# Kernel tuning notes

Hardware: AMD Instinct MI355X
Metric: run time of the kernel (lower is better)

## Reference

```python
import jax, jax.numpy as jnp
import numpy as np
import math

B, T, C, H = 2, 2048, 1024, 16
D = C // H

def setup_inputs() -> dict:
    key = jax.random.key(0)
    ks = jax.random.split(key, 10)
    s = 1.0 / math.sqrt(C)
    return {
        "x": jax.random.normal(ks[0], (B, T, C), jnp.float32),
        "x_query": jax.random.normal(ks[1], (B, T, C), jnp.float32),
        "Wq": jax.random.normal(ks[2], (C, C), jnp.float32) * s,
        "bq": jax.random.normal(ks[3], (C,), jnp.float32) * 0.02,
        "Wk": jax.random.normal(ks[4], (C, C), jnp.float32) * s,
        "bk": jax.random.normal(ks[5], (C,), jnp.float32) * 0.02,
        "Wv": jax.random.normal(ks[6], (C, C), jnp.float32) * s,
        "bv": jax.random.normal(ks[7], (C,), jnp.float32) * 0.02,
        "Wp": jax.random.normal(ks[8], (C, C), jnp.float32) * s,
        "bp": jax.random.normal(ks[9], (C,), jnp.float32) * 0.02,
    }

def reference(x, x_query, Wq, bq, Wk, bk, Wv, bv, Wp, bp):
    # torch nn.Linear: y = x @ W^T + b
    Tq = x_query.shape[1]
    Tk = x.shape[1]
    q = (x_query @ Wq.T + bq).reshape(B, Tq, H, D).transpose(0, 2, 1, 3)  # [B,H,Tq,D]
    k = (x @ Wk.T + bk).reshape(B, Tk, H, D).transpose(0, 2, 1, 3)       # [B,H,Tk,D]
    v = (x @ Wv.T + bv).reshape(B, Tk, H, D).transpose(0, 2, 1, 3)       # [B,H,Tk,D]
    scale = 1.0 / math.sqrt(D)
    att = jnp.einsum('bhqd,bhkd->bhqk', q, k) * scale                    # [B,H,Tq,Tk]
    # use_mask=True, past_kv=None -> causal tril mask over (Tq, Tk)
    mask = jnp.tril(jnp.ones((Tq, Tk), dtype=bool))
    att = jnp.where(mask[None, None, :, :], att, -jnp.inf)
    att = jax.nn.softmax(att, axis=-1)
    y = jnp.einsum('bhqk,bhkd->bhqd', att, v)                            # [B,H,Tq,D]
    y = y.transpose(0, 2, 1, 3).reshape(B, Tq, C)
    y = y @ Wp.T + bp
    return y
```

## Files before the change

kernel.cpp:

```cpp
#include <hip/hip_runtime.h>

typedef __bf16 bf16;
typedef __attribute__((ext_vector_type(8))) __bf16 bf16x8;
typedef __attribute__((ext_vector_type(4))) float f32x4;
typedef __attribute__((ext_vector_type(16))) float f32x16;
typedef __attribute__((ext_vector_type(4))) unsigned u32x4;

#define MFMA16(a, b, c) __builtin_amdgcn_mfma_f32_16x16x32_bf16((a), (b), (c), 0, 0, 0)
#define MFMA32(a, b, c) __builtin_amdgcn_mfma_f32_32x32x16_bf16((a), (b), (c), 0, 0, 0)
#define NEG_BIG (-1e30f)
#define SCL_LOG2 0.18033688011112042f
#define THR_RAW 44.3614195558365f

__device__ __forceinline__ void gload_lds16(void* lds, const void* g) {
  __builtin_amdgcn_global_load_lds(
      (const __attribute__((address_space(1))) void*)g,
      (__attribute__((address_space(3))) void*)lds, 16, 0, 0);
}

__device__ __forceinline__ unsigned pk2(float x, float y) {
  const unsigned short a = __builtin_bit_cast(unsigned short, (bf16)x);
  const unsigned short b = __builtin_bit_cast(unsigned short, (bf16)y);
  return (unsigned)a | ((unsigned)b << 16);
}

static __device__ const signed char KQT[32] =
  {15,15,10,10, 15,14,14,14,13, 9, 9, 4, 13,13,12,12, 8, 8,
   12,11,11,11, 7, 7, 3,  6, 6,  5, 5, 2,  1,  0};
static __device__ const signed char KSEG[32] =
  { 0, 1, 0, 1,  2, 0, 1, 2, 0, 0, 1, 0,  1, 2, 0, 1, 0, 1,
    2, 0, 1, 2, 0, 1, 0,  0, 1,  0, 1, 0,  0,  0};

__global__ void cvt6(const float* __restrict__ s0, const float* __restrict__ s1,
                     const float* __restrict__ s2, const float* __restrict__ s3,
                     const float* __restrict__ s4, const float* __restrict__ s5,
                     bf16* __restrict__ d0, bf16* __restrict__ d1,
                     bf16* __restrict__ d2, bf16* __restrict__ d3,
                     bf16* __restrict__ d4, bf16* __restrict__ d5) {
  const int c = blockIdx.x * blockDim.x + threadIdx.x;
  if (c >= 1572864) return;
  const float* s; bf16* d; int off;
  if (c < 524288)        { s = s0; d = d0; off = c; }
  else if (c < 1048576)  { s = s1; d = d1; off = c - 524288; }
  else {
    const int c2 = c - 1048576, seg = c2 >> 17;
    off = c2 & 131071;
    s = seg == 0 ? s2 : seg == 1 ? s3 : seg == 2 ? s4 : s5;
    d = seg == 0 ? d2 : seg == 1 ? d3 : seg == 2 ? d4 : d5;
  }
  const float4 a = ((const float4*)s)[off * 2 + 0];
  const float4 b = ((const float4*)s)[off * 2 + 1];
  bf16x8 o;
  o[0] = (bf16)a.x; o[1] = (bf16)a.y; o[2] = (bf16)a.z; o[3] = (bf16)a.w;
  o[4] = (bf16)b.x; o[5] = (bf16)b.y; o[6] = (bf16)b.z; o[7] = (bf16)b.w;
  ((bf16x8*)d)[off] = o;
}

__global__ void gemm_qkv(const bf16* __restrict__ XQ, const bf16* __restrict__ X,
                         const bf16* __restrict__ Wq, const bf16* __restrict__ Wk,
                         const bf16* __restrict__ Wv,
                         const float* __restrict__ bq, const float* __restrict__ bk,
                         const float* __restrict__ bv,
                         bf16* __restrict__ Qo, bf16* __restrict__ Ko,
                         bf16* __restrict__ Vto) {
  __shared__ __align__(16) char As[128 * 128];
  __shared__ __align__(16) char Bs[128 * 128];
  const int tid = threadIdx.x;
  const int wv = tid >> 6, lane = tid & 63;
  const int wr = wv >> 1, wc = wv & 1;
  const int lr = lane & 15, lg = lane >> 4;
  const int seg = blockIdx.x >> 3;
  const int n0 = (blockIdx.x & 7) * 128;
  const int m0 = blockIdx.y * 128;
  const bf16* __restrict__ A = seg == 0 ? XQ : X;
  const bf16* __restrict__ W = seg == 0 ? Wq : seg == 1 ? Wk : Wv;
  const float* __restrict__ bias = seg == 0 ? bq : seg == 1 ? bk : bv;
  const int K = 1024;

  f32x4 acc[4][4] = {};

  for (int k0 = 0; k0 < K; k0 += 64) {
    __syncthreads();
#pragma unroll
    for (int j = 0; j < 4; ++j) {
      const int c = j * 256 + tid;
      const int row = c >> 3, cc = c & 7;
      const int gcol = (cc ^ (row & 7)) * 8;
      gload_lds16(As + (j * 256 + wv * 64) * 16,
                  A + (size_t)(m0 + row) * K + k0 + gcol);
      gload_lds16(Bs + (j * 256 + wv * 64) * 16,
                  W + (size_t)(n0 + row) * K + k0 + gcol);
    }
    __syncthreads();
#pragma unroll
    for (int half = 0; half < 2; ++half) {
      const int kb = half * 64 + lg * 16;
      bf16x8 af[4], bfr[4];
#pragma unroll
      for (int i = 0; i < 4; ++i) {
        const int row = wr * 64 + i * 16 + lr;
        af[i] = *(const bf16x8*)(As + row * 128 + (kb ^ ((row & 7) << 4)));
      }
#pragma unroll
      for (int j = 0; j < 4; ++j) {
        const int row = wc * 64 + j * 16 + lr;
        bfr[j] = *(const bf16x8*)(Bs + row * 128 + (kb ^ ((row & 7) << 4)));
      }
#pragma unroll
      for (int i = 0; i < 4; ++i)
#pragma unroll
        for (int j = 0; j < 4; ++j)
          acc[i][j] = MFMA16(af[i], bfr[j], acc[i][j]);
    }
  }

#pragma unroll
  for (int j = 0; j < 4; ++j) {
    const int n = n0 + wc * 64 + j * 16 + lr;
    const float bvv = bias[n];
    const int h = n >> 6, d = n & 63;
#pragma unroll
    for (int i = 0; i < 4; ++i) {
#pragma unroll
      for (int r = 0; r < 4; ++r) {
        const int m = m0 + wr * 64 + i * 16 + lg * 4 + r;
        const float v = acc[i][j][r] + bvv;
        const int b = m >> 11, t = m & 2047;
        if (seg == 0)      Qo[((size_t)(b * 16 + h) * 2048 + t) * 64 + d] = (bf16)v;
        else if (seg == 1) Ko[((size_t)(b * 16 + h) * 2048 + t) * 64 + d] = (bf16)v;
        else               Vto[((size_t)(b * 16 + h) * 64 + d) * 2048 + t] = (bf16)v;
      }
    }
  }
}

__global__ void gemm_out(const bf16* __restrict__ A, const bf16* __restrict__ W,
                         const float* __restrict__ bias, float* __restrict__ out,
                         int M, int N, int K) {
  __shared__ __align__(16) char As[128 * 128];
  __shared__ __align__(16) char Bs[64 * 128];
  const int tid = threadIdx.x;
  const int wv = tid >> 6, lane = tid & 63;
  const int wr = wv >> 1, wc = wv & 1;
  const int lr = lane & 15, lg = lane >> 4;
  const int m0 = blockIdx.y * 128, n0 = blockIdx.x * 64;

  f32x4 acc[4][2] = {};

  for (int k0 = 0; k0 < K; k0 += 64) {
    __syncthreads();
#pragma unroll
    for (int j = 0; j < 4; ++j) {
      const int c = j * 256 + tid;
      const int row = c >> 3, cc = c & 7;
      const int gcol = (cc ^ (row & 7)) * 8;
      gload_lds16(As + (j * 256 + wv * 64) * 16,
                  A + (size_t)(m0 + row) * K + k0 + gcol);
    }
#pragma unroll
    for (int j = 0; j < 2; ++j) {
      const int c = j * 256 + tid;
      const int row = c >> 3, cc = c & 7;
      const int gcol = (cc ^ (row & 7)) * 8;
      gload_lds16(Bs + (j * 256 + wv * 64) * 16,
                  W + (size_t)(n0 + row) * K + k0 + gcol);
    }
    __syncthreads();
#pragma unroll
    for (int half = 0; half < 2; ++half) {
      const int kb = half * 64 + lg * 16;
      bf16x8 af[4], bfr[2];
#pragma unroll
      for (int i = 0; i < 4; ++i) {
        const int row = wr * 64 + i * 16 + lr;
        af[i] = *(const bf16x8*)(As + row * 128 + (kb ^ ((row & 7) << 4)));
      }
#pragma unroll
      for (int j = 0; j < 2; ++j) {
        const int row = wc * 32 + j * 16 + lr;
        bfr[j] = *(const bf16x8*)(Bs + row * 128 + (kb ^ ((row & 7) << 4)));
      }
#pragma unroll
      for (int i = 0; i < 4; ++i)
#pragma unroll
        for (int j = 0; j < 2; ++j)
          acc[i][j] = MFMA16(af[i], bfr[j], acc[i][j]);
    }
  }

#pragma unroll
  for (int j = 0; j < 2; ++j) {
    const int n = n0 + wc * 32 + j * 16 + lr;
    const float bv = bias[n];
#pragma unroll
    for (int i = 0; i < 4; ++i) {
#pragma unroll
      for (int r = 0; r < 4; ++r) {
        const int m = m0 + wr * 64 + i * 16 + lg * 4 + r;
        out[(size_t)m * N + n] = acc[i][j][r] + bv;
      }
    }
  }
}

__global__ void attn_fwd(const bf16* __restrict__ Q, const bf16* __restrict__ Kk,
                         const bf16* __restrict__ Vt, bf16* __restrict__ attout,
                         bf16* __restrict__ Opart, float* __restrict__ Ml) {
  __shared__ __align__(16) char Ks[2][8192];
  __shared__ __align__(16) char Vs[2][8192];

  const int tid = threadIdx.x;
  const int wv = tid >> 6, lane = tid & 63;
  const int q31 = lane & 31, hi = lane >> 5, l7 = lane & 7;
  const int kind = blockIdx.x >> 5, bh = blockIdx.x & 31;
  const int qt = KQT[kind], seg = KSEG[kind];
  const int nt = 2 * qt + 2;
  const int ns = qt >= 11 ? 3 : (qt >= 5 ? 2 : 1);
  const int t0 = (nt * seg) / ns, t1 = (nt * (seg + 1)) / ns;
  const bool split = ns > 1;

  const int q0 = qt * 128;
  const int qs = q0 + wv * 32;
  const int qa = qs + q31;
  const size_t bhT = (size_t)bh * 2048;
  const bf16* Vh = Vt + (size_t)bh * 64 * 2048;

  bf16x8 qf[4];
#pragma unroll
  for (int kw = 0; kw < 4; ++kw)
    qf[kw] = *(const bf16x8*)(Q + (bhT + qa) * 64 + kw * 16 + hi * 8);

  u32x4 onesu; onesu[0] = onesu[1] = onesu[2] = onesu[3] = 0x3F803F80u;
  const bf16x8 ones8 = __builtin_bit_cast(bf16x8, onesu);

  f32x16 O0 = {}, O1 = {};
  f32x16 Ol = {};
  float m2 = NEG_BIG;

  auto STAGE = [&](int buf, int kv0) {
#pragma unroll
    for (int rr = 0; rr < 2; ++rr) {
      const int c = rr * 256 + tid;
      const int row = c >> 3, cc = c & 7;
      const int gcol = (cc ^ (row & 7)) * 8;
      gload_lds16(Ks[buf] + (rr * 256 + wv * 64) * 16,
                  Kk + (bhT + kv0 + row) * 64 + gcol);
      gload_lds16(Vs[buf] + (rr * 256 + wv * 64) * 16,
                  Vh + (size_t)row * 2048 + kv0 + gcol);
    }
  };

  STAGE(0, t0 * 64);
  __syncthreads();

  for (int it = t0; it < t1; ++it) {
    const int kv0 = it * 64;
    const int cur = (it - t0) & 1;
    if (it + 1 < t1) STAGE(cur ^ 1, (it + 1) * 64);

    if (kv0 <= qs + 31) {
      f32x16 S0 = {}, S1 = {};
      __builtin_amdgcn_s_setprio(1);
#pragma unroll
      for (int kw = 0; kw < 4; ++kw) {
        const int cb = (32 * kw + 16 * hi) ^ (l7 << 4);
        const bf16x8 k0 = *(const bf16x8*)(Ks[cur] + q31 * 128 + cb);
        const bf16x8 k1 = *(const bf16x8*)(Ks[cur] + (32 + q31) * 128 + cb);
        S0 = MFMA32(k0, qf[kw], S0);
        S1 = MFMA32(k1, qf[kw], S1);
      }
      __builtin_amdgcn_s_setprio(0);

      float p[32];
#pragma unroll
      for (int r = 0; r < 16; ++r) { p[r] = S0[r]; p[16 + r] = S1[r]; }
      if (kv0 + 63 > qs) {
#pragma unroll
        for (int a = 0; a < 2; ++a)
#pragma unroll
          for (int r = 0; r < 16; ++r) {
            const int kva = kv0 + a * 32 + (r & 3) + 8 * (r >> 2) + 4 * hi;
            if (kva > qa) p[a * 16 + r] = NEG_BIG;
          }
      }

      float w16[16];
#pragma unroll
      for (int i = 0; i < 16; ++i) w16[i] = fmaxf(p[i], p[i + 16]);
#pragma unroll
      for (int i = 0; i < 8; ++i) w16[i] = fmaxf(w16[i], w16[i + 8]);
#pragma unroll
      for (int i = 0; i < 4; ++i) w16[i] = fmaxf(w16[i], w16[i + 4]);
      float mx = fmaxf(fmaxf(w16[0], w16[1]), fmaxf(w16[2], w16[3]));
      mx = fmaxf(mx, __shfl_xor(mx, 32));
      if (!__all(mx - m2 <= THR_RAW)) {
        const float mnew = fmaxf(m2, mx);
        const float fac = exp2f((m2 - mnew) * SCL_LOG2);
#pragma unroll
        for (int r = 0; r < 16; ++r) { O0[r] *= fac; O1[r] *= fac; }
        Ol[0] *= fac;
        m2 = mnew;
      }
      const float nm2 = -m2 * SCL_LOG2;
#pragma unroll
      for (int i = 0; i < 32; ++i) p[i] = exp2f(__builtin_fmaf(p[i], SCL_LOG2, nm2));

      bf16x8 pf[4];
#pragma unroll
      for (int ks = 0; ks < 4; ++ks) {
        const int base = 16 * (ks >> 1) + 8 * (ks & 1);
        const unsigned g0 = pk2(p[base + 0], p[base + 1]);
        const unsigned g1 = pk2(p[base + 2], p[base + 3]);
        const unsigned g2 = pk2(p[base + 4], p[base + 5]);
        const unsigned g3 = pk2(p[base + 6], p[base + 7]);
        const unsigned e0 = __shfl_xor(hi ? g0 : g2, 32);
        const unsigned e1 = __shfl_xor(hi ? g1 : g3, 32);
        u32x4 w4;
        w4[0] = hi ? e0 : g0;
        w4[1] = hi ? e1 : g1;
        w4[2] = hi ? g2 : e0;
        w4[3] = hi ? g3 : e1;
        pf[ks] = __builtin_bit_cast(bf16x8, w4);
      }

      __builtin_amdgcn_s_setprio(1);
#pragma unroll
      for (int ks = 0; ks < 4; ++ks) {
        const int cb = (32 * ks + 16 * hi) ^ (l7 << 4);
        const bf16x8 v0 = *(const bf16x8*)(Vs[cur] + q31 * 128 + cb);
        const bf16x8 v1 = *(const bf16x8*)(Vs[cur] + (32 + q31) * 128 + cb);
        O0 = MFMA32(v0, pf[ks], O0);
        O1 = MFMA32(v1, pf[ks], O1);
        Ol = MFMA32(ones8, pf[ks], Ol);
      }
      __builtin_amdgcn_s_setprio(0);
    }
    __syncthreads();
  }

  const float l = Ol[0];
  if (!split) {
    const int b = bh >> 4, h = bh & 15;
    const float inv = 1.f / l;
    bf16* orow = attout + ((size_t)b * 2048 + qa) * 1024 + h * 64;
#pragma unroll
    for (int r = 0; r < 16; ++r) {
      const int dd = (r & 3) + 8 * (r >> 2) + 4 * hi;
      orow[dd]      = (bf16)(O0[r] * inv);
      orow[32 + dd] = (bf16)(O1[r] * inv);
    }
  } else {
    const int sbase = (qt < 11) ? (qt - 5) * 2 : 12 + (qt - 11) * 3;
    const int slot = bh * 27 + sbase + seg;
    bf16* Po = Opart + (size_t)slot * 8192;
    const int row = wv * 32 + q31;
#pragma unroll
    for (int r = 0; r < 16; ++r) {
      const int dd = (r & 3) + 8 * (r >> 2) + 4 * hi;
      Po[row * 64 + dd]      = (bf16)O0[r];
      Po[row * 64 + 32 + dd] = (bf16)O1[r];
    }
    Ml[slot * 256 + row]       = m2;
    Ml[slot * 256 + 128 + row] = l;
  }
}

__global__ void attn_combine(const bf16* __restrict__ Opart,
                             const float* __restrict__ Ml,
                             bf16* __restrict__ attout) {
  const int u = blockIdx.x;
  const int bh = u / 11, qti = u - bh * 11;
  const int qt = qti + 5;
  const int ns = qt >= 11 ? 3 : 2;
  const int sbase = (qt < 11) ? (qt - 5) * 2 : 12 + (qt - 11) * 3;
  const int s0 = bh * 27 + sbase;
  const int tid = threadIdx.x;
  const int row = tid >> 1, c0 = (tid & 1) * 32;

  float m[3], lv[3];
  float M = NEG_BIG;
#pragma unroll
  for (int s = 0; s < 3; ++s)
    if (s < ns) {
      m[s] = Ml[(s0 + s) * 256 + row];
      lv[s] = Ml[(s0 + s) * 256 + 128 + row];
      M = fmaxf(M, m[s]);
    }
  float w[3], L = 0.f;
#pragma unroll
  for (int s = 0; s < 3; ++s)
    if (s < ns) {
      w[s] = exp2f((m[s] - M) * SCL_LOG2);
      L += w[s] * lv[s];
    }
  const float inv = 1.f / L;

  float acc[32] = {};
#pragma unroll
  for (int s = 0; s < 3; ++s)
    if (s < ns) {
      const bf16* p = Opart + (size_t)(s0 + s) * 8192 + row * 64 + c0;
      const float ws = w[s];
#pragma unroll
      for (int j = 0; j < 4; ++j) {
        const bf16x8 v = *(const bf16x8*)(p + j * 8);
#pragma unroll
        for (int e = 0; e < 8; ++e) acc[j * 8 + e] += ws * (float)v[e];
      }
    }

  const int b = bh >> 4, h = bh & 15, t = qt * 128 + row;
  bf16* dst = attout + ((size_t)b * 2048 + t) * 1024 + h * 64 + c0;
#pragma unroll
  for (int d = 0; d < 32; ++d) dst[d] = (bf16)(acc[d] * inv);
}

extern "C" void kernel_launch(void* const* d_in, const int* in_sizes, int n_in,
                              void* d_out, int out_size, void* d_ws, size_t ws_size,
                              hipStream_t stream) {
  const float* x   = (const float*)d_in[0];
  const float* xq  = (const float*)d_in[1];
  const float* Wq  = (const float*)d_in[2];
  const float* bq  = (const float*)d_in[3];
  const float* Wk  = (const float*)d_in[4];
  const float* bk  = (const float*)d_in[5];
  const float* Wv  = (const float*)d_in[6];
  const float* bv  = (const float*)d_in[7];
  const float* Wp  = (const float*)d_in[8];
  const float* bp  = (const float*)d_in[9];
  float* out = (float*)d_out;

  const size_t NTC = 4194304;
  const size_t NW  = 1048576;
  bf16* ws = (bf16*)d_ws;
  bf16* XQb = ws;
  bf16* Xb  = XQb + NTC;
  bf16* Wqb = Xb + NTC;
  bf16* Wkb = Wqb + NW;
  bf16* Wvb = Wkb + NW;
  bf16* Wpb = Wvb + NW;
  bf16* Qw  = Wpb + NW;
  bf16* Kw  = Qw + NTC;
  bf16* Vtw = Kw + NTC;
  bf16* Aw  = Vtw + NTC;
  bf16* Opart = (bf16*)d_ws;
  float* Ml   = (float*)(Aw + NTC);

  dim3 blk(256);
  cvt6<<<dim3(6144), blk, 0, stream>>>(xq, x, Wq, Wk, Wv, Wp,
                                       XQb, Xb, Wqb, Wkb, Wvb, Wpb);
  gemm_qkv<<<dim3(24, 32), blk, 0, stream>>>(XQb, Xb, Wqb, Wkb, Wvb,
                                             bq, bk, bv, Qw, Kw, Vtw);
  attn_fwd<<<dim3(1024), blk, 0, stream>>>(Qw, Kw, Vtw, Aw, Opart, Ml);
  attn_combine<<<dim3(352), blk, 0, stream>>>(Opart, Ml, Aw);
  gemm_out<<<dim3(16, 32), blk, 0, stream>>>(Aw, Wpb, bp, out, 4096, 1024, 1024);
}
```

Baseline: 118.6 us.

## Software-pipeline QK^T one tile ahead of softmax and PV in attention

Splits K and V staging so K is prefetched two tiles ahead and V one tile ahead. The QK^T MFMAs for the next tile are issued before the current tile's softmax and PV, letting matrix work overlap the exp and shuffle work. It also adds launch bounds of 256 threads with 4 blocks per CU. The cost is more live accumulator registers (two extra f32x16), which with the occupancy hint may cause spills. Buffer indexing switches to it&1 and the K buffer is refilled two tiles ahead.

```diff
diff --git a/kernel.cpp b/kernel.cpp
--- a/kernel.cpp
+++ b/kernel.cpp
@@ -203,9 +203,10 @@
   }
 }
 
-__global__ void attn_fwd(const bf16* __restrict__ Q, const bf16* __restrict__ Kk,
-                         const bf16* __restrict__ Vt, bf16* __restrict__ attout,
-                         bf16* __restrict__ Opart, float* __restrict__ Ml) {
+__global__ void __launch_bounds__(256, 4)
+attn_fwd(const bf16* __restrict__ Q, const bf16* __restrict__ Kk,
+         const bf16* __restrict__ Vt, bf16* __restrict__ attout,
+         bf16* __restrict__ Opart, float* __restrict__ Ml) {
   __shared__ __align__(16) char Ks[2][8192];
   __shared__ __align__(16) char Vs[2][8192];
 
@@ -237,7 +238,7 @@
   f32x16 Ol = {};
   float m2 = NEG_BIG;
 
-  auto STAGE = [&](int buf, int kv0) {
+  auto STAGE_K = [&](int buf, int kv0) {
 #pragma unroll
     for (int rr = 0; rr < 2; ++rr) {
       const int c = rr * 256 + tid;
@@ -245,48 +246,75 @@
       const int gcol = (cc ^ (row & 7)) * 8;
       gload_lds16(Ks[buf] + (rr * 256 + wv * 64) * 16,
                   Kk + (bhT + kv0 + row) * 64 + gcol);
+    }
+  };
+  auto STAGE_V = [&](int buf, int kv0) {
+#pragma unroll
+    for (int rr = 0; rr < 2; ++rr) {
+      const int c = rr * 256 + tid;
+      const int row = c >> 3, cc = c & 7;
+      const int gcol = (cc ^ (row & 7)) * 8;
       gload_lds16(Vs[buf] + (rr * 256 + wv * 64) * 16,
                   Vh + (size_t)row * 2048 + kv0 + gcol);
     }
   };
-
-  STAGE(0, t0 * 64);
+  auto QKT = [&](int kbuf, f32x16& A0, f32x16& A1) {
+    __builtin_amdgcn_s_setprio(1);
+#pragma unroll
+    for (int kw = 0; kw < 4; ++kw) {
+      const int cb = (32 * kw + 16 * hi) ^ (l7 << 4);
+      const bf16x8 k0 = *(const bf16x8*)(Ks[kbuf] + q31 * 128 + cb);
+      const bf16x8 k1 = *(const bf16x8*)(Ks[kbuf] + (32 + q31) * 128 + cb);
+      A0 = MFMA32(k0, qf[kw], A0);
+      A1 = MFMA32(k1, qf[kw], A1);
+    }
+    __builtin_amdgcn_s_setprio(0);
+  };
+  auto mk_pf = [&](float a0, float a1, float a2, float a3,
+                   float a4, float a5, float a6, float a7) -> bf16x8 {
+    const unsigned g0 = pk2(a0, a1), g1 = pk2(a2, a3);
+    const unsigned g2 = pk2(a4, a5), g3 = pk2(a6, a7);
+    const unsigned e0 = __shfl_xor(hi ? g0 : g2, 32);
+    const unsigned e1 = __shfl_xor(hi ? g1 : g3, 32);
+    u32x4 w4;
+    w4[0] = hi ? e0 : g0;
+    w4[1] = hi ? e1 : g1;
+    w4[2] = hi ? g2 : e0;
+    w4[3] = hi ? g3 : e1;
+    return __builtin_bit_cast(bf16x8, w4);
+  };
+
+  STAGE_K(t0 & 1, t0 * 64);
+  if (t0 + 1 < t1) STAGE_K((t0 + 1) & 1, (t0 + 1) * 64);
+  STAGE_V(t0 & 1, t0 * 64);
+  __syncthreads();
+
+  f32x16 S0 = {}, S1 = {};
+  if (t0 * 64 <= qs + 31) QKT(t0 & 1, S0, S1);
   __syncthreads();
 
   for (int it = t0; it < t1; ++it) {
     const int kv0 = it * 64;
-    const int cur = (it - t0) & 1;
-    if (it + 1 < t1) STAGE(cur ^ 1, (it + 1) * 64);
+    if (it + 2 < t1) STAGE_K(it & 1, (it + 2) * 64);
+    if (it + 1 < t1) STAGE_V((it + 1) & 1, (it + 1) * 64);
+
+    f32x16 N0 = {}, N1 = {};
+    const bool nx = (it + 1 < t1) && ((it + 1) * 64 <= qs + 31);
+    if (nx) QKT((it + 1) & 1, N0, N1);
 
     if (kv0 <= qs + 31) {
-      f32x16 S0 = {}, S1 = {};
-      __builtin_amdgcn_s_setprio(1);
-#pragma unroll
-      for (int kw = 0; kw < 4; ++kw) {
-        const int cb = (32 * kw + 16 * hi) ^ (l7 << 4);
-        const bf16x8 k0 = *(const bf16x8*)(Ks[cur] + q31 * 128 + cb);
-        const bf16x8 k1 = *(const bf16x8*)(Ks[cur] + (32 + q31) * 128 + cb);
-        S0 = MFMA32(k0, qf[kw], S0);
-        S1 = MFMA32(k1, qf[kw], S1);
-      }
-      __builtin_amdgcn_s_setprio(0);
-
-      float p[32];
-#pragma unroll
-      for (int r = 0; r < 16; ++r) { p[r] = S0[r]; p[16 + r] = S1[r]; }
       if (kv0 + 63 > qs) {
 #pragma unroll
-        for (int a = 0; a < 2; ++a)
-#pragma unroll
-          for (int r = 0; r < 16; ++r) {
-            const int kva = kv0 + a * 32 + (r & 3) + 8 * (r >> 2) + 4 * hi;
-            if (kva > qa) p[a * 16 + r] = NEG_BIG;
-          }
+        for (int r = 0; r < 16; ++r) {
+          const int kva = kv0 + (r & 3) + 8 * (r >> 2) + 4 * hi;
+          if (kva > qa)      S0[r] = NEG_BIG;
+          if (kva + 32 > qa) S1[r] = NEG_BIG;
+        }
       }
 
       float w16[16];
 #pragma unroll
-      for (int i = 0; i < 16; ++i) w16[i] = fmaxf(p[i], p[i + 16]);
+      for (int i = 0; i < 16; ++i) w16[i] = fmaxf(S0[i], S1[i]);
 #pragma unroll
       for (int i = 0; i < 8; ++i) w16[i] = fmaxf(w16[i], w16[i + 8]);
 #pragma unroll
@@ -303,32 +331,24 @@
       }
       const float nm2 = -m2 * SCL_LOG2;
 #pragma unroll
-      for (int i = 0; i < 32; ++i) p[i] = exp2f(__builtin_fmaf(p[i], SCL_LOG2, nm2));
+      for (int i = 0; i < 16; ++i)
+        S0[i] = exp2f(__builtin_fmaf(S0[i], SCL_LOG2, nm2));
+#pragma unroll
+      for (int i = 0; i < 16; ++i)
+        S1[i] = exp2f(__builtin_fmaf(S1[i], SCL_LOG2, nm2));
 
       bf16x8 pf[4];
-#pragma unroll
-      for (int ks = 0; ks < 4; ++ks) {
-        const int base = 16 * (ks >> 1) + 8 * (ks & 1);
-        const unsigned g0 = pk2(p[base + 0], p[base + 1]);
-        const unsigned g1 = pk2(p[base + 2], p[base + 3]);
-        const unsigned g2 = pk2(p[base + 4], p[base + 5]);
-        const unsigned g3 = pk2(p[base + 6], p[base + 7]);
-        const unsigned e0 = __shfl_xor(hi ? g0 : g2, 32);
-        const unsigned e1 = __shfl_xor(hi ? g1 : g3, 32);
-        u32x4 w4;
-        w4[0] = hi ? e0 : g0;
-        w4[1] = hi ? e1 : g1;
-        w4[2] = hi ? g2 : e0;
-        w4[3] = hi ? g3 : e1;
-        pf[ks] = __builtin_bit_cast(bf16x8, w4);
-      }
+      pf[0] = mk_pf(S0[0], S0[1], S0[2], S0[3], S0[4], S0[5], S0[6], S0[7]);
+      pf[1] = mk_pf(S0[8], S0[9], S0[10], S0[11], S0[12], S0[13], S0[14], S0[15]);
+      pf[2] = mk_pf(S1[0], S1[1], S1[2], S1[3], S1[4], S1[5], S1[6], S1[7]);
+      pf[3] = mk_pf(S1[8], S1[9], S1[10], S1[11], S1[12], S1[13], S1[14], S1[15]);
 
       __builtin_amdgcn_s_setprio(1);
 #pragma unroll
       for (int ks = 0; ks < 4; ++ks) {
         const int cb = (32 * ks + 16 * hi) ^ (l7 << 4);
-        const bf16x8 v0 = *(const bf16x8*)(Vs[cur] + q31 * 128 + cb);
-        const bf16x8 v1 = *(const bf16x8*)(Vs[cur] + (32 + q31) * 128 + cb);
+        const bf16x8 v0 = *(const bf16x8*)(Vs[it & 1] + q31 * 128 + cb);
+        const bf16x8 v1 = *(const bf16x8*)(Vs[it & 1] + (32 + q31) * 128 + cb);
         O0 = MFMA32(v0, pf[ks], O0);
         O1 = MFMA32(v1, pf[ks], O1);
         Ol = MFMA32(ones8, pf[ks], Ol);
@@ -336,6 +356,7 @@
       __builtin_amdgcn_s_setprio(0);
     }
     __syncthreads();
+    S0 = N0; S1 = N1;
   }
 
   const float l = Ol[0];
```

Measured after the change: 219.3 us. 84.9% more time.

## Triple-buffer K tiles and prefetch K two iterations ahead in attention

Applied to the files above, without the earlier changes.

Splits the K/V staging so K tiles are triple-buffered and fetched two iterations ahead, while V stays double-buffered one ahead. The end-of-iteration __syncthreads is replaced by a partial vmcnt wait plus s_barrier, so the newest K loads can remain in flight across the barrier. This aims to hide global-to-LDS latency for the QK^T stage. It costs an extra 8KB of LDS per block, which may lower occupancy.

```diff
diff --git a/kernel.cpp b/kernel.cpp
--- a/kernel.cpp
+++ b/kernel.cpp
@@ -206,7 +206,7 @@
 __global__ void attn_fwd(const bf16* __restrict__ Q, const bf16* __restrict__ Kk,
                          const bf16* __restrict__ Vt, bf16* __restrict__ attout,
                          bf16* __restrict__ Opart, float* __restrict__ Ml) {
-  __shared__ __align__(16) char Ks[2][8192];
+  __shared__ __align__(16) char Ks[3][8192];
   __shared__ __align__(16) char Vs[2][8192];
 
   const int tid = threadIdx.x;
@@ -237,7 +237,7 @@
   f32x16 Ol = {};
   float m2 = NEG_BIG;
 
-  auto STAGE = [&](int buf, int kv0) {
+  auto STAGE_K = [&](int buf, int kv0) {
 #pragma unroll
     for (int rr = 0; rr < 2; ++rr) {
       const int c = rr * 256 + tid;
@@ -245,18 +245,30 @@
       const int gcol = (cc ^ (row & 7)) * 8;
       gload_lds16(Ks[buf] + (rr * 256 + wv * 64) * 16,
                   Kk + (bhT + kv0 + row) * 64 + gcol);
+    }
+  };
+  auto STAGE_V = [&](int buf, int kv0) {
+#pragma unroll
+    for (int rr = 0; rr < 2; ++rr) {
+      const int c = rr * 256 + tid;
+      const int row = c >> 3, cc = c & 7;
+      const int gcol = (cc ^ (row & 7)) * 8;
       gload_lds16(Vs[buf] + (rr * 256 + wv * 64) * 16,
                   Vh + (size_t)row * 2048 + kv0 + gcol);
     }
   };
 
-  STAGE(0, t0 * 64);
-  __syncthreads();
+  STAGE_V(t0 % 2, t0 * 64);
+  STAGE_K(t0 % 3, t0 * 64);
+  if (t0 + 1 < t1) STAGE_K((t0 + 1) % 3, (t0 + 1) * 64);
+  asm volatile("s_waitcnt vmcnt(0)" ::: "memory");
+  __builtin_amdgcn_s_barrier();
+  __builtin_amdgcn_sched_barrier(0);
 
   for (int it = t0; it < t1; ++it) {
     const int kv0 = it * 64;
-    const int cur = (it - t0) & 1;
-    if (it + 1 < t1) STAGE(cur ^ 1, (it + 1) * 64);
+    if (it + 1 < t1) STAGE_V((it + 1) % 2, (it + 1) * 64);
+    if (it + 2 < t1) STAGE_K((it + 2) % 3, (it + 2) * 64);
 
     if (kv0 <= qs + 31) {
       f32x16 S0 = {}, S1 = {};
@@ -264,8 +276,8 @@
 #pragma unroll
       for (int kw = 0; kw < 4; ++kw) {
         const int cb = (32 * kw + 16 * hi) ^ (l7 << 4);
-        const bf16x8 k0 = *(const bf16x8*)(Ks[cur] + q31 * 128 + cb);
-        const bf16x8 k1 = *(const bf16x8*)(Ks[cur] + (32 + q31) * 128 + cb);
+        const bf16x8 k0 = *(const bf16x8*)(Ks[it % 3] + q31 * 128 + cb);
+        const bf16x8 k1 = *(const bf16x8*)(Ks[it % 3] + (32 + q31) * 128 + cb);
         S0 = MFMA32(k0, qf[kw], S0);
         S1 = MFMA32(k1, qf[kw], S1);
       }
@@ -327,15 +339,24 @@
 #pragma unroll
       for (int ks = 0; ks < 4; ++ks) {
         const int cb = (32 * ks + 16 * hi) ^ (l7 << 4);
-        const bf16x8 v0 = *(const bf16x8*)(Vs[cur] + q31 * 128 + cb);
-        const bf16x8 v1 = *(const bf16x8*)(Vs[cur] + (32 + q31) * 128 + cb);
+        const bf16x8 v0 = *(const bf16x8*)(Vs[it % 2] + q31 * 128 + cb);
+        const bf16x8 v1 = *(const bf16x8*)(Vs[it % 2] + (32 + q31) * 128 + cb);
         O0 = MFMA32(v0, pf[ks], O0);
         O1 = MFMA32(v1, pf[ks], O1);
         Ol = MFMA32(ones8, pf[ks], Ol);
       }
       __builtin_amdgcn_s_setprio(0);
     }
-    __syncthreads();
+
+    if (it + 1 < t1) {
+      if (it + 2 < t1) {
+        asm volatile("s_waitcnt vmcnt(2)" ::: "memory");
+      } else {
+        asm volatile("s_waitcnt vmcnt(0)" ::: "memory");
+      }
+      __builtin_amdgcn_s_barrier();
+      __builtin_amdgcn_sched_barrier(0);
+    }
   }
 
   const float l = Ol[0];
```

New measurement: 121.0 us. No clear change (+2.0%).
